# Optimization experiments

Hardware: AMD Instinct MI355X
Metric: run time of the kernel (lower is better)

Reference implementation:

```python
import jax, jax.numpy as jnp
import numpy as np

H = 8          # n_heads
DK = 128       # d_model // h
D = H * DK     # d_model = 1024
B, S = 8, 1024
D_LIST = (32, 64, 96, 128)  # sorted set of hidden//h from config dict


def setup_inputs() -> dict:
    key = jax.random.key(0)
    ks = jax.random.split(key, 13)
    mk = lambda k, shape: jax.random.normal(k, shape, dtype=jnp.float32)
    inp = {
        'query': mk(ks[0], (B, S, D)),
        'key': mk(ks[1], (B, S, D)),
        'value': mk(ks[2], (B, S, D)),
        'config_idx': jax.random.randint(ks[3], (B,), 0, len(D_LIST), dtype=jnp.int32),
        'Wq': mk(ks[4], (D, D)) * 0.02, 'bq': jnp.zeros((D,), jnp.float32),
        'Wk': mk(ks[5], (D, D)) * 0.02, 'bk': jnp.zeros((D,), jnp.float32),
        'Wv': mk(ks[6], (D, D)) * 0.02, 'bv': jnp.zeros((D,), jnp.float32),
        'Wo': mk(ks[7], (D, D)) * 0.02, 'bo': jnp.zeros((D,), jnp.float32),
    }
    return inp


def _mha_arrange(query, key, value, config_idx, Wq, bq, Wk, bk, Wv, bv, Wo, bo):
    Bb, Ss, _ = query.shape
    proj = lambda x, W, b: (x @ W.T + b).reshape(Bb, Ss, H, DK).transpose(0, 2, 1, 3)
    q = proj(query, Wq, bq)   # [B,H,S,DK]
    k = proj(key, Wk, bk)
    v = proj(value, Wv, bv)
    scores = jnp.einsum('bhqd,bhkd->bhqk', q, k) / np.float32(np.sqrt(DK))
    p = jax.nn.softmax(scores, axis=-1)
    ctx = jnp.einsum('bhqk,bhkd->bhqd', p, v).transpose(0, 2, 1, 3)  # [B,S,H,DK]
    # attn_arrange: per-sample width d; pack first d dims of each head densely
    ret = jnp.zeros((Bb, Ss, H * DK), query.dtype)
    for i, d in enumerate(D_LIST):
        packed = ctx[:, :, :, :d].reshape(Bb, Ss, H * d)           # [B,S,H*d]
        packed = jnp.pad(packed, ((0, 0), (0, 0), (0, H * (DK - d))))
        sel = (config_idx == i)[:, None, None]
        ret = ret + jnp.where(sel, packed, jnp.zeros((), query.dtype))
    return ret @ Wo.T + bo


def reference(query, key, value, config_idx, Wq, bq, Wk, bk, Wv, bv, Wo, bo):
    return _mha_arrange(query, key, value, config_idx, Wq, bq, Wk, bk, Wv, bv, Wo, bo)
```

## Files before the change

### kernel.cpp

```cpp
#include <hip/hip_runtime.h>
#include <hip/hip_bf16.h>


typedef __attribute__((ext_vector_type(8))) __bf16 bf16x8;
typedef __attribute__((ext_vector_type(4))) float f32x4;

#define DEV static __device__ __forceinline__

DEV float exp2v(float x) { return __builtin_amdgcn_exp2f(x); }

DEV unsigned short f2bf(float f) {
  union { float f; unsigned int u; } c; c.f = f;
  unsigned int u = c.u + 0x7fffu + ((c.u >> 16) & 1u);
  return (unsigned short)(u >> 16);
}

DEV unsigned cvtpk(float a, float b) {
  unsigned r;
  asm("v_cvt_pk_bf16_f32 %0, %1, %2" : "=v"(r) : "v"(a), "v"(b));
  return r;
}

DEV void gload16(const void* g, void* l) {
  __builtin_amdgcn_global_load_lds((const __attribute__((address_space(1))) void*)g,
                                   (__attribute__((address_space(3))) void*)l, 16, 0, 0);
}

#define LGKM0 asm volatile("s_waitcnt lgkmcnt(0)" ::: "memory")
#define BAR   __builtin_amdgcn_s_barrier()
#define VMC6  asm volatile("s_waitcnt vmcnt(6)" ::: "memory")
#define VMC0  asm volatile("s_waitcnt vmcnt(0)" ::: "memory")

DEV void cv4(const float* __restrict__ s, unsigned short* __restrict__ d, int i) {
  const float4 a = *(const float4*)(s + i);
  ushort4 o;
  o.x = f2bf(a.x); o.y = f2bf(a.y); o.z = f2bf(a.z); o.w = f2bf(a.w);
  *(ushort4*)(d + i) = o;
}

__global__ __launch_bounds__(256) void convert_kernel(
    const float* __restrict__ q, const float* __restrict__ k, const float* __restrict__ v,
    const float* __restrict__ wq, const float* __restrict__ wk,
    const float* __restrict__ wv, const float* __restrict__ wo,
    unsigned short* __restrict__ xq, unsigned short* __restrict__ xk,
    unsigned short* __restrict__ xv, unsigned short* __restrict__ wb)
{
  const int i = (blockIdx.x * 256 + threadIdx.x) * 4;
  cv4(q, xq, i);
  cv4(k, xk, i);
  cv4(v, xv, i);
  if (i < 4 * 1024 * 1024) {
    const int which = i >> 20, off = i & 1048575;
    const float* s = which == 0 ? wq : which == 1 ? wk : which == 2 ? wv : wo;
    cv4(s, wb + (which << 20), off);
  }
}

template<int OUTMODE>
__global__ __launch_bounds__(512, 1) void gemmS(
    const unsigned short* __restrict__ xq, const unsigned short* __restrict__ xk,
    const unsigned short* __restrict__ xv, const unsigned short* __restrict__ wb,
    const float* __restrict__ bq, const float* __restrict__ bk,
    const float* __restrict__ bv,
    unsigned short* __restrict__ Qp, unsigned short* __restrict__ Kp,
    unsigned short* __restrict__ VTp, float* __restrict__ fout)
{
  __shared__ __align__(16) char LDS[147456];
  int z, mt, nt;
  if (OUTMODE == 0) {
    const int swz = (blockIdx.x & 7) * 96 + (blockIdx.x >> 3);
    z = swz >> 8; const int rem = swz & 255; mt = rem >> 3; nt = rem & 7;
  } else {
    const int swz = (blockIdx.x & 7) * 32 + (blockIdx.x >> 3);
    z = 0; mt = swz >> 3; nt = swz & 7;
  }
  const int m0 = mt * 256, n0 = nt * 128;
  const unsigned short* Ag = (OUTMODE == 1) ? xq : (z == 0 ? xq : z == 1 ? xk : xv);
  const unsigned short* Bg = (OUTMODE == 1) ? wb : wb + ((size_t)z << 20);
  const float* bias = (OUTMODE == 1) ? bq : (z == 0 ? bq : z == 1 ? bk : bv);

  const int tid = threadIdx.x, lane = tid & 63, w = tid >> 6;
  const int wm = w >> 1, wn = w & 1;
  const int g = lane >> 4, ln = lane & 15;

  const f32x4 fzero = {0.f, 0.f, 0.f, 0.f};
  f32x4 acc[4][4];
#pragma unroll
  for (int i = 0; i < 4; i++)
#pragma unroll
    for (int j = 0; j < 4; j++) acc[i][j] = fzero;

  bf16x8 bfr[4][2];
  bf16x8 afr[4][2];

  auto SA = [&](int bf, int hf, int k0) {
    const unsigned short* src = Ag + (size_t)(m0 + hf * 128) * 1024 + k0;
    char* base = LDS + bf * 32768 + hf * 16384 + w * 2048;
#pragma unroll
    for (int r2 = 0; r2 < 2; ++r2) {
      const int o = w * 2048 + r2 * 1024 + lane * 16;
      const int rwi = o >> 7, cb = o & 127;
      gload16(src + (size_t)rwi * 1024 + ((cb ^ ((rwi & 7) << 4)) >> 1), base + r2 * 1024);
    }
  };
  auto SB = [&](int bf, int k0) {
    const unsigned short* src = Bg + (size_t)n0 * 1024 + k0;
    char* base = LDS + 98304 + bf * 16384 + w * 2048;
#pragma unroll
    for (int r2 = 0; r2 < 2; ++r2) {
      const int o = w * 2048 + r2 * 1024 + lane * 16;
      const int rwi = o >> 7, cb = o & 127;
      gload16(src + (size_t)rwi * 1024 + ((cb ^ ((rwi & 7) << 4)) >> 1), base + r2 * 1024);
    }
  };
  auto rdA = [&](int bf, int q) {
#pragma unroll
    for (int p = 0; p < 2; ++p) {
      const int row = wm * 64 + (2 * q + p) * 16 + ln;
      const int sw = (row & 7) << 4;
#pragma unroll
      for (int kc = 0; kc < 2; ++kc)
        afr[2 * q + p][kc] = *(const bf16x8*)(LDS + bf * 32768 + row * 128 + ((kc * 64 + g * 16) ^ sw));
    }
  };
  auto rdB = [&](int bf) {
#pragma unroll
    for (int nf = 0; nf < 4; ++nf) {
      const int row = wn * 64 + nf * 16 + ln;
      const int sw = (row & 7) << 4;
#pragma unroll
      for (int kc = 0; kc < 2; ++kc)
        bfr[nf][kc] = *(const bf16x8*)(LDS + 98304 + bf * 16384 + row * 128 + ((kc * 64 + g * 16) ^ sw));
    }
  };
  auto mm = [&](int q) {
    __builtin_amdgcn_s_setprio(1);
#pragma unroll
    for (int p = 0; p < 2; ++p)
#pragma unroll
      for (int nf = 0; nf < 4; ++nf)
#pragma unroll
        for (int kc = 0; kc < 2; ++kc)
          acc[2 * q + p][nf] =
              __builtin_amdgcn_mfma_f32_16x16x32_bf16(afr[2 * q + p][kc], bfr[nf][kc],
                                                      acc[2 * q + p][nf], 0, 0, 0);
    __builtin_amdgcn_s_setprio(0);
  };

  SA(0, 0, 0); SA(0, 1, 0); SB(0, 0);
  SA(1, 0, 64); SA(1, 1, 64); SB(1, 64);
  VMC6; BAR;

  int br = 0, bw = 2;
  for (int t = 0; t < 16; ++t) {
    const int kL = (t + 2) << 6;
    rdB(br); rdA(br, 0); rdA(br, 1);
    if (t < 14) { SA(bw, 0, kL); SA(bw, 1, kL); SB(bw, kL); }
    BAR; LGKM0;
    mm(0); mm(1);
    if (t < 14) { VMC6; } else if (t == 14) { VMC0; }
    BAR;
    br = br == 2 ? 0 : br + 1;
    bw = bw == 2 ? 0 : bw + 1;
  }

  const float QS = 0.12751743f;
#pragma unroll
  for (int mf = 0; mf < 4; ++mf)
#pragma unroll
    for (int nf = 0; nf < 4; ++nf) {
      const int m = m0 + wm * 64 + mf * 16 + g * 4;
      const int n = n0 + wn * 64 + nf * 16 + ln;
      const float bn = bias[n];
      if (OUTMODE == 1) {
#pragma unroll
        for (int r = 0; r < 4; ++r)
          fout[(size_t)(m + r) * 1024 + n] = acc[mf][nf][r] + bn;
      } else if (z == 0) {
#pragma unroll
        for (int r = 0; r < 4; ++r)
          Qp[(size_t)(m + r) * 1024 + n] = f2bf((acc[mf][nf][r] + bn) * QS);
      } else if (z == 1) {
#pragma unroll
        for (int r = 0; r < 4; ++r)
          Kp[(size_t)(m + r) * 1024 + n] = f2bf(acc[mf][nf][r] + bn);
      } else {
        const int b = m >> 10, s0 = m & 1023;
        uint2 pk;
        pk.x = cvtpk(acc[mf][nf][0] + bn, acc[mf][nf][1] + bn);
        pk.y = cvtpk(acc[mf][nf][2] + bn, acc[mf][nf][3] + bn);
        *(uint2*)(VTp + (((size_t)(b * 1024 + n)) << 10) + s0) = pk;
      }
    }
}

__global__ __launch_bounds__(512) void attn_kernel(
    const unsigned short* __restrict__ Qp, const unsigned short* __restrict__ Kp,
    const unsigned short* __restrict__ VT, const int* __restrict__ cfg,
    unsigned short* __restrict__ ret)
{
  __shared__ __align__(16) unsigned short Ks[2][64 * 128];
  __shared__ __align__(16) unsigned short Vs[2][128 * 64];
  __shared__ __align__(16) unsigned short Ps[8 * 16 * 64];
  const int bx = blockIdx.x;
  const int qb = bx >> 6, bh = bx & 63, b = bh >> 3, h = bh & 7;
  const int tid = threadIdx.x, lane = tid & 63, w = tid >> 6;
  const int g = lane >> 4, ln = lane & 15;
  const int q0 = qb * 128;
  const f32x4 fzero = {0.f, 0.f, 0.f, 0.f};

  bf16x8 qf[4];
  {
    const unsigned short* qrow = Qp + ((size_t)(b * 1024 + q0 + w * 16 + ln)) * 1024 + h * 128;
#pragma unroll
    for (int kc = 0; kc < 4; kc++) qf[kc] = *(const bf16x8*)(qrow + kc * 32 + g * 8);
  }
  float m_run = -1e30f, l_run = 0.f;
  f32x4 o_acc[8];
#pragma unroll
  for (int i = 0; i < 8; i++) o_acc[i] = fzero;

  auto stage = [&](int buf, int kv0) {
#pragma unroll
    for (int i = 0; i < 2; ++i) {
      const int o = i * 8192 + tid * 16;
      {
        const int r = o >> 8, cb = o & 255;
        const int cs = cb ^ ((r & 7) << 4);
        gload16(Kp + ((size_t)(b * 1024 + kv0 + r)) * 1024 + h * 128 + (cs >> 1),
                (char*)Ks + buf * 16384 + o);
      }
      {
        const int r = o >> 7, cb = o & 127;
        const int cs = cb ^ ((r & 7) << 4);
        gload16(VT + ((size_t)((b * 8 + h) * 128 + r)) * 1024 + kv0 + (cs >> 1),
                (char*)Vs + buf * 16384 + o);
      }
    }
  };

  stage(0, 0);
  asm volatile("s_waitcnt vmcnt(0)" ::: "memory");
  __syncthreads();

  int cur = 0;
  for (int t = 0; t < 16; ++t) {
    if (t < 15) stage(cur ^ 1, (t + 1) * 64);

    f32x4 sc[4];
    __builtin_amdgcn_s_setprio(1);
#pragma unroll
    for (int nb = 0; nb < 4; ++nb) {
      sc[nb] = fzero;
      const int rr = nb * 16 + ln;
      const int sw = (rr & 7) << 4;
#pragma unroll
      for (int kc = 0; kc < 4; ++kc) {
        const bf16x8 kf = *(const bf16x8*)((const char*)Ks + cur * 16384 + rr * 256 +
                                           (((kc * 32 + g * 8) << 1) ^ sw));
        sc[nb] = __builtin_amdgcn_mfma_f32_16x16x32_bf16(kf, qf[kc], sc[nb], 0, 0, 0);
      }
    }
    __builtin_amdgcn_s_setprio(0);

    float mnb[4];
#pragma unroll
    for (int nb = 0; nb < 4; ++nb)
      mnb[nb] = fmaxf(fmaxf(sc[nb][0], sc[nb][1]), fmaxf(sc[nb][2], sc[nb][3]));
    float pmax = fmaxf(fmaxf(mnb[0], mnb[1]), fmaxf(mnb[2], mnb[3]));
    pmax = fmaxf(pmax, __shfl_xor(pmax, 16));
    pmax = fmaxf(pmax, __shfl_xor(pmax, 32));
    if (__any(pmax > m_run + 11.5f)) {
      const float mnew = fmaxf(m_run, pmax);
      const float alpha = exp2v(m_run - mnew);
      l_run *= alpha;
      m_run = mnew;
      float ar[4];
#pragma unroll
      for (int r = 0; r < 4; ++r)
        ar[r] = __shfl(alpha, (lane & 48) | (((lane >> 4) & 3) << 2) | r);
#pragma unroll
      for (int i = 0; i < 8; i++)
#pragma unroll
        for (int r = 0; r < 4; r++) o_acc[i][r] *= ar[r];
    }
    float sum = 0.f;
    float pvv[16];
#pragma unroll
    for (int nb = 0; nb < 4; ++nb)
#pragma unroll
      for (int r = 0; r < 4; ++r) {
        const float p = exp2v(sc[nb][r] - m_run);
        pvv[nb * 4 + r] = p; sum += p;
      }
    l_run += sum;

    {
      char* pbase = (char*)Ps + w * 2048 + ln * 128;
#pragma unroll
      for (int nb = 0; nb < 4; ++nb) {
        uint2 pk;
        pk.x = cvtpk(pvv[nb * 4 + 0], pvv[nb * 4 + 1]);
        pk.y = cvtpk(pvv[nb * 4 + 2], pvv[nb * 4 + 3]);
        *(uint2*)(pbase + (((16 * nb + 4 * g) << 1) ^ ((ln & 7) << 4))) = pk;
      }
    }
    bf16x8 pf[2];
#pragma unroll
    for (int kc = 0; kc < 2; kc++)
      pf[kc] = *(const bf16x8*)((const char*)Ps + w * 2048 + ln * 128 +
                                (((kc * 32 + g * 8) << 1) ^ ((ln & 7) << 4)));

    __builtin_amdgcn_s_setprio(1);
#pragma unroll
    for (int nb2 = 0; nb2 < 8; ++nb2) {
      const int rr = nb2 * 16 + ln;
      const int sw = (rr & 7) << 4;
#pragma unroll
      for (int kc = 0; kc < 2; ++kc) {
        const bf16x8 vf = *(const bf16x8*)((const char*)Vs + cur * 16384 + rr * 128 +
                                           (((kc * 32 + g * 8) << 1) ^ sw));
        o_acc[nb2] = __builtin_amdgcn_mfma_f32_16x16x32_bf16(pf[kc], vf, o_acc[nb2], 0, 0, 0);
      }
    }
    __builtin_amdgcn_s_setprio(0);

    if (t < 15) {
      asm volatile("s_waitcnt vmcnt(0)" ::: "memory");
      __syncthreads();
    }
    cur ^= 1;
  }

  l_run += __shfl_xor(l_run, 16);
  l_run += __shfl_xor(l_run, 32);
  float rl[4];
#pragma unroll
  for (int r = 0; r < 4; ++r)
    rl[r] = 1.0f / __shfl(l_run, (lane & 48) | (((lane >> 4) & 3) << 2) | r);
  const int d_b = 32 * (cfg[b] + 1);
  const int zw = 128 - d_b;
  const size_t rowbase = (size_t)(b * 1024 + q0 + w * 16 + g * 4);
#pragma unroll
  for (int nb2 = 0; nb2 < 8; ++nb2) {
    const int dk = nb2 * 16 + ln;
    if (dk < d_b) {
#pragma unroll
      for (int r = 0; r < 4; r++)
        ret[(rowbase + r) * 1024 + h * d_b + dk] = f2bf(o_acc[nb2][r] * rl[r]);
    } else {
#pragma unroll
      for (int r = 0; r < 4; r++)
        ret[(rowbase + r) * 1024 + 8 * d_b + h * zw + (dk - d_b)] = 0;
    }
  }
}

extern "C" void kernel_launch(void* const* d_in, const int* in_sizes, int n_in,
                              void* d_out, int out_size, void* d_ws, size_t ws_size,
                              hipStream_t stream)
{
  (void)in_sizes; (void)n_in; (void)out_size; (void)ws_size;
  const float* q   = (const float*)d_in[0];
  const float* k   = (const float*)d_in[1];
  const float* v   = (const float*)d_in[2];
  const int*   cfg = (const int*)d_in[3];
  const float* Wq  = (const float*)d_in[4];  const float* bq = (const float*)d_in[5];
  const float* Wk  = (const float*)d_in[6];  const float* bk = (const float*)d_in[7];
  const float* Wv  = (const float*)d_in[8];  const float* bv = (const float*)d_in[9];
  const float* Wo  = (const float*)d_in[10]; const float* bo = (const float*)d_in[11];

  const size_t X  = 8192ull * 1024ull;
  const size_t WN = 1024ull * 1024ull;
  char* p = (char*)d_ws;
  unsigned short* xq  = (unsigned short*)p; p += X * 2;
  unsigned short* xk  = (unsigned short*)p; p += X * 2;
  unsigned short* xv  = (unsigned short*)p; p += X * 2;
  unsigned short* wb  = (unsigned short*)p; p += 4 * WN * 2;
  unsigned short* Qp  = (unsigned short*)p; p += X * 2;
  unsigned short* Kp  = (unsigned short*)p; p += X * 2;
  unsigned short* VTp = (unsigned short*)p; p += X * 2;
  unsigned short* ret = (unsigned short*)p; p += X * 2;

  convert_kernel<<<dim3(8192), dim3(256), 0, stream>>>(q, k, v, Wq, Wk, Wv, Wo,
                                                       xq, xk, xv, wb);

  gemmS<0><<<dim3(768), dim3(512), 0, stream>>>(xq, xk, xv, wb, bq, bk, bv,
                                                Qp, Kp, VTp, nullptr);

  attn_kernel<<<dim3(512), dim3(512), 0, stream>>>(Qp, Kp, VTp, cfg, ret);

  gemmS<1><<<dim3(256), dim3(512), 0, stream>>>(ret, nullptr, nullptr, wb + 3 * WN,
                                                bo, nullptr, nullptr,
                                                nullptr, nullptr, nullptr,
                                                (float*)d_out);
}
```

Measured before the change: 171.0 us.

## Fuse fp32-to-bf16 activation conversion into QKV projection GEMM loads

The separate pass that converted the query, key and value activations to bf16 is removed. The QKV GEMM now streams fp32 activations straight into LDS and converts them to bf16 at fragment-read time. The M tile is halved to 128 so the fp32 A tile fits, which doubles the grid to 1536 blocks. This drops a full read-and-write round trip over the 3x32MB activations, at the cost of twice the A-side load bytes per tile, more conversion ALU work inside the main loop, and less reuse per block.

```diff
diff --git a/kernel.cpp b/kernel.cpp
--- a/kernel.cpp
+++ b/kernel.cpp
@@ -38,63 +38,175 @@
   *(ushort4*)(d + i) = o;
 }
 
-__global__ __launch_bounds__(256) void convert_kernel(
-    const float* __restrict__ q, const float* __restrict__ k, const float* __restrict__ v,
+__global__ __launch_bounds__(256) void convert_w(
     const float* __restrict__ wq, const float* __restrict__ wk,
     const float* __restrict__ wv, const float* __restrict__ wo,
-    unsigned short* __restrict__ xq, unsigned short* __restrict__ xk,
-    unsigned short* __restrict__ xv, unsigned short* __restrict__ wb)
+    unsigned short* __restrict__ wb)
 {
   const int i = (blockIdx.x * 256 + threadIdx.x) * 4;
-  cv4(q, xq, i);
-  cv4(k, xk, i);
-  cv4(v, xv, i);
-  if (i < 4 * 1024 * 1024) {
-    const int which = i >> 20, off = i & 1048575;
-    const float* s = which == 0 ? wq : which == 1 ? wk : which == 2 ? wv : wo;
-    cv4(s, wb + (which << 20), off);
-  }
-}
-
-template<int OUTMODE>
-__global__ __launch_bounds__(512, 1) void gemmS(
-    const unsigned short* __restrict__ xq, const unsigned short* __restrict__ xk,
-    const unsigned short* __restrict__ xv, const unsigned short* __restrict__ wb,
+  const int which = i >> 20, off = i & 1048575;
+  const float* s = which == 0 ? wq : which == 1 ? wk : which == 2 ? wv : wo;
+  cv4(s, wb + (which << 20), off);
+}
+
+__global__ __launch_bounds__(512, 1) void gemmF(
+    const float* __restrict__ Aq, const float* __restrict__ Ak,
+    const float* __restrict__ Av, const unsigned short* __restrict__ wb,
     const float* __restrict__ bq, const float* __restrict__ bk,
     const float* __restrict__ bv,
     unsigned short* __restrict__ Qp, unsigned short* __restrict__ Kp,
-    unsigned short* __restrict__ VTp, float* __restrict__ fout)
+    unsigned short* __restrict__ VTp)
 {
   __shared__ __align__(16) char LDS[147456];
-  int z, mt, nt;
-  if (OUTMODE == 0) {
-    const int swz = (blockIdx.x & 7) * 96 + (blockIdx.x >> 3);
-    z = swz >> 8; const int rem = swz & 255; mt = rem >> 3; nt = rem & 7;
-  } else {
-    const int swz = (blockIdx.x & 7) * 32 + (blockIdx.x >> 3);
-    z = 0; mt = swz >> 3; nt = swz & 7;
-  }
-  const int m0 = mt * 256, n0 = nt * 128;
-  const unsigned short* Ag = (OUTMODE == 1) ? xq : (z == 0 ? xq : z == 1 ? xk : xv);
-  const unsigned short* Bg = (OUTMODE == 1) ? wb : wb + ((size_t)z << 20);
-  const float* bias = (OUTMODE == 1) ? bq : (z == 0 ? bq : z == 1 ? bk : bv);
+  const int swz = (blockIdx.x & 7) * 192 + (blockIdx.x >> 3);
+  const int z = swz >> 9;
+  const int rem = swz & 511;
+  const int mt = rem >> 3, nt = rem & 7;
+  const int m0 = mt * 128, n0 = nt * 128;
+  const float* Af = z == 0 ? Aq : z == 1 ? Ak : Av;
+  const unsigned short* Bg = wb + ((size_t)z << 20);
+  const float* bias = z == 0 ? bq : z == 1 ? bk : bv;
 
   const int tid = threadIdx.x, lane = tid & 63, w = tid >> 6;
   const int wm = w >> 1, wn = w & 1;
   const int g = lane >> 4, ln = lane & 15;
 
   const f32x4 fzero = {0.f, 0.f, 0.f, 0.f};
+  f32x4 acc[2][4];
+#pragma unroll
+  for (int i = 0; i < 2; i++)
+#pragma unroll
+    for (int j = 0; j < 4; j++) acc[i][j] = fzero;
+
+  bf16x8 bfr[4][2], afr[2][2];
+
+  auto SA = [&](int bf, int k0) {
+#pragma unroll
+    for (int i = 0; i < 4; ++i) {
+      const int o = i * 8192 + tid * 16;
+      const int row = o >> 8, cb = o & 255;
+      gload16(Af + (size_t)(m0 + row) * 1024 + k0 + ((cb ^ ((row & 7) << 5)) >> 2),
+              LDS + bf * 32768 + o);
+    }
+  };
+  auto SB = [&](int bf, int k0) {
+#pragma unroll
+    for (int i = 0; i < 2; ++i) {
+      const int o = i * 8192 + tid * 16;
+      const int row = o >> 7, cb = o & 127;
+      gload16(Bg + (size_t)(n0 + row) * 1024 + k0 + ((cb ^ ((row & 7) << 4)) >> 1),
+              LDS + 98304 + bf * 16384 + o);
+    }
+  };
+  auto rdA = [&](int bf) {
+#pragma unroll
+    for (int p = 0; p < 2; ++p) {
+      const int row = wm * 32 + p * 16 + ln;
+      const int sw = (row & 7) << 5;
+#pragma unroll
+      for (int kc = 0; kc < 2; ++kc) {
+        const int c = (kc * 128 + g * 32) ^ sw;
+        const char* base = LDS + bf * 32768 + row * 256;
+        const f32x4 lo = *(const f32x4*)(base + c);
+        const f32x4 hi = *(const f32x4*)(base + c + 16);
+        union { unsigned u[4]; bf16x8 v; } cv;
+        cv.u[0] = cvtpk(lo[0], lo[1]); cv.u[1] = cvtpk(lo[2], lo[3]);
+        cv.u[2] = cvtpk(hi[0], hi[1]); cv.u[3] = cvtpk(hi[2], hi[3]);
+        afr[p][kc] = cv.v;
+      }
+    }
+  };
+  auto rdB = [&](int bf) {
+#pragma unroll
+    for (int nf = 0; nf < 4; ++nf) {
+      const int row = wn * 64 + nf * 16 + ln;
+      const int sw = (row & 7) << 4;
+#pragma unroll
+      for (int kc = 0; kc < 2; ++kc)
+        bfr[nf][kc] = *(const bf16x8*)(LDS + 98304 + bf * 16384 + row * 128 +
+                                       ((kc * 64 + g * 16) ^ sw));
+    }
+  };
+  auto mm = [&]() {
+    __builtin_amdgcn_s_setprio(1);
+#pragma unroll
+    for (int p = 0; p < 2; ++p)
+#pragma unroll
+      for (int nf = 0; nf < 4; ++nf)
+#pragma unroll
+        for (int kc = 0; kc < 2; ++kc)
+          acc[p][nf] = __builtin_amdgcn_mfma_f32_16x16x32_bf16(afr[p][kc], bfr[nf][kc],
+                                                               acc[p][nf], 0, 0, 0);
+    __builtin_amdgcn_s_setprio(0);
+  };
+
+  SA(0, 0); SB(0, 0);
+  SA(1, 64); SB(1, 64);
+  VMC6; BAR;
+
+  int br = 0, bw = 2;
+  for (int t = 0; t < 16; ++t) {
+    const int kL = (t + 2) << 6;
+    rdA(br); rdB(br);
+    if (t < 14) { SA(bw, kL); SB(bw, kL); }
+    BAR; LGKM0;
+    mm();
+    if (t < 14) { VMC6; } else if (t == 14) { VMC0; }
+    BAR;
+    br = br == 2 ? 0 : br + 1;
+    bw = bw == 2 ? 0 : bw + 1;
+  }
+
+  const float QS = 0.12751743f;
+#pragma unroll
+  for (int mf = 0; mf < 2; ++mf)
+#pragma unroll
+    for (int nf = 0; nf < 4; ++nf) {
+      const int m = m0 + wm * 32 + mf * 16 + g * 4;
+      const int n = n0 + wn * 64 + nf * 16 + ln;
+      const float bn = bias[n];
+      if (z == 0) {
+#pragma unroll
+        for (int r = 0; r < 4; ++r)
+          Qp[(size_t)(m + r) * 1024 + n] = f2bf((acc[mf][nf][r] + bn) * QS);
+      } else if (z == 1) {
+#pragma unroll
+        for (int r = 0; r < 4; ++r)
+          Kp[(size_t)(m + r) * 1024 + n] = f2bf(acc[mf][nf][r] + bn);
+      } else {
+        const int b = m >> 10, s0 = m & 1023;
+        uint2 pk;
+        pk.x = cvtpk(acc[mf][nf][0] + bn, acc[mf][nf][1] + bn);
+        pk.y = cvtpk(acc[mf][nf][2] + bn, acc[mf][nf][3] + bn);
+        *(uint2*)(VTp + (((size_t)(b * 1024 + n)) << 10) + s0) = pk;
+      }
+    }
+}
+
+__global__ __launch_bounds__(512, 1) void gemm_out(
+    const unsigned short* __restrict__ Abf, const unsigned short* __restrict__ Bg,
+    const float* __restrict__ bias, float* __restrict__ fout)
+{
+  __shared__ __align__(16) char LDS[147456];
+  const int swz = (blockIdx.x & 7) * 32 + (blockIdx.x >> 3);
+  const int mt = swz >> 3, nt = swz & 7;
+  const int m0 = mt * 256, n0 = nt * 128;
+
+  const int tid = threadIdx.x, lane = tid & 63, w = tid >> 6;
+  const int wm = w >> 1, wn = w & 1;
+  const int g = lane >> 4, ln = lane & 15;
+
+  const f32x4 fzero = {0.f, 0.f, 0.f, 0.f};
   f32x4 acc[4][4];
 #pragma unroll
   for (int i = 0; i < 4; i++)
 #pragma unroll
     for (int j = 0; j < 4; j++) acc[i][j] = fzero;
 
-  bf16x8 bfr[4][2];
-  bf16x8 afr[4][2];
+  bf16x8 bfr[4][2], afr[4][2];
 
   auto SA = [&](int bf, int hf, int k0) {
-    const unsigned short* src = Ag + (size_t)(m0 + hf * 128) * 1024 + k0;
+    const unsigned short* src = Abf + (size_t)(m0 + hf * 128) * 1024 + k0;
     char* base = LDS + bf * 32768 + hf * 16384 + w * 2048;
 #pragma unroll
     for (int r2 = 0; r2 < 2; ++r2) {
@@ -164,7 +276,6 @@
     bw = bw == 2 ? 0 : bw + 1;
   }
 
-  const float QS = 0.12751743f;
 #pragma unroll
   for (int mf = 0; mf < 4; ++mf)
 #pragma unroll
@@ -172,25 +283,9 @@
       const int m = m0 + wm * 64 + mf * 16 + g * 4;
       const int n = n0 + wn * 64 + nf * 16 + ln;
       const float bn = bias[n];
-      if (OUTMODE == 1) {
-#pragma unroll
-        for (int r = 0; r < 4; ++r)
-          fout[(size_t)(m + r) * 1024 + n] = acc[mf][nf][r] + bn;
-      } else if (z == 0) {
-#pragma unroll
-        for (int r = 0; r < 4; ++r)
-          Qp[(size_t)(m + r) * 1024 + n] = f2bf((acc[mf][nf][r] + bn) * QS);
-      } else if (z == 1) {
-#pragma unroll
-        for (int r = 0; r < 4; ++r)
-          Kp[(size_t)(m + r) * 1024 + n] = f2bf(acc[mf][nf][r] + bn);
-      } else {
-        const int b = m >> 10, s0 = m & 1023;
-        uint2 pk;
-        pk.x = cvtpk(acc[mf][nf][0] + bn, acc[mf][nf][1] + bn);
-        pk.y = cvtpk(acc[mf][nf][2] + bn, acc[mf][nf][3] + bn);
-        *(uint2*)(VTp + (((size_t)(b * 1024 + n)) << 10) + s0) = pk;
-      }
+#pragma unroll
+      for (int r = 0; r < 4; ++r)
+        fout[(size_t)(m + r) * 1024 + n] = acc[mf][nf][r] + bn;
     }
 }
 
@@ -373,25 +468,18 @@
   const size_t X  = 8192ull * 1024ull;
   const size_t WN = 1024ull * 1024ull;
   char* p = (char*)d_ws;
-  unsigned short* xq  = (unsigned short*)p; p += X * 2;
-  unsigned short* xk  = (unsigned short*)p; p += X * 2;
-  unsigned short* xv  = (unsigned short*)p; p += X * 2;
   unsigned short* wb  = (unsigned short*)p; p += 4 * WN * 2;
   unsigned short* Qp  = (unsigned short*)p; p += X * 2;
   unsigned short* Kp  = (unsigned short*)p; p += X * 2;
   unsigned short* VTp = (unsigned short*)p; p += X * 2;
   unsigned short* ret = (unsigned short*)p; p += X * 2;
 
-  convert_kernel<<<dim3(8192), dim3(256), 0, stream>>>(q, k, v, Wq, Wk, Wv, Wo,
-                                                       xq, xk, xv, wb);
-
-  gemmS<0><<<dim3(768), dim3(512), 0, stream>>>(xq, xk, xv, wb, bq, bk, bv,
-                                                Qp, Kp, VTp, nullptr);
+  convert_w<<<dim3(4096), dim3(256), 0, stream>>>(Wq, Wk, Wv, Wo, wb);
+
+  gemmF<<<dim3(1536), dim3(512), 0, stream>>>(q, k, v, wb, bq, bk, bv,
+                                              Qp, Kp, VTp);
 
   attn_kernel<<<dim3(512), dim3(512), 0, stream>>>(Qp, Kp, VTp, cfg, ret);
 
-  gemmS<1><<<dim3(256), dim3(512), 0, stream>>>(ret, nullptr, nullptr, wb + 3 * WN,
-                                                bo, nullptr, nullptr,
-                                                nullptr, nullptr, nullptr,
-                                                (float*)d_out);
-}
+  gemm_out<<<dim3(256), dim3(512), 0, stream>>>(ret, wb + 3 * WN, bo, (float*)d_out);
+}
```

Measured after the change: 183.5 us. +7.3%, slower.
